# Kernel tuning notes

Measured on AMD Instinct MI355X. Metric: run time of the kernel, lower is better.

Reference implementation:

```python
import jax, jax.numpy as jnp
import numpy as np

N = 100000   # nodes
E = 3200000  # edges (avg degree 32)
G = 512      # graphs in batch
IN = 128     # in_channels
H1, C1 = 8, 8  # conv1 heads, per-head channels
OUT = 64     # out_channels (conv2, 1 head)
NEG_SLOPE = 0.2


def setup_inputs() -> dict:
    key = jax.random.key(0)
    ks = jax.random.split(key, 12)
    s = 0.1
    return dict(
        x=jax.random.normal(ks[0], (N, IN), jnp.float32),
        edge_index=jax.random.randint(ks[1], (2, E), 0, N),
        batch=jnp.sort(jax.random.randint(ks[2], (N,), 0, G)),
        W1=jax.random.normal(ks[3], (IN, H1 * C1), jnp.float32) * s,
        att_src1=jax.random.normal(ks[4], (H1, C1), jnp.float32) * s,
        att_dst1=jax.random.normal(ks[5], (H1, C1), jnp.float32) * s,
        b1=jnp.zeros((H1 * C1,), jnp.float32),
        W2=jax.random.normal(ks[6], (H1 * C1, OUT), jnp.float32) * s,
        att_src2=jax.random.normal(ks[7], (1, OUT), jnp.float32) * s,
        att_dst2=jax.random.normal(ks[8], (1, OUT), jnp.float32) * s,
        b2=jnp.zeros((OUT,), jnp.float32),
        lw1=jax.random.normal(ks[9], (OUT, 128), jnp.float32) * s,
        lb1=jnp.zeros((128,), jnp.float32),
        lw2=jax.random.normal(ks[10], (128, 1), jnp.float32) * s,
        lb2=jnp.zeros((1,), jnp.float32),
    )


def gat_layer(x, src, dst, W, a_src, a_dst, bias, heads, outc):
    # PyG GATConv (eval mode): linear -> per-edge leaky_relu attention ->
    # segment softmax over incoming edges per dst -> weighted scatter-add.
    n = x.shape[0]
    h = (x @ W).reshape(n, heads, outc)                      # [N,H,C]
    a_s = jnp.einsum('nhc,hc->nh', h, a_src)                 # [N,H]
    a_d = jnp.einsum('nhc,hc->nh', h, a_dst)
    e = jax.nn.leaky_relu(a_s[src] + a_d[dst], NEG_SLOPE)    # [E',H]
    m = jax.ops.segment_max(e, dst, num_segments=n)
    m = jax.lax.stop_gradient(jnp.where(jnp.isfinite(m), m, 0.0))
    ex = jnp.exp(e - m[dst])
    denom = jax.ops.segment_sum(ex, dst, num_segments=n)
    alpha = ex / jnp.maximum(denom[dst], 1e-16)              # [E',H]
    out = jax.ops.segment_sum(h[src] * alpha[:, :, None], dst, num_segments=n)
    return out.reshape(n, heads * outc) + bias


def reference(x, W1, att_src1, att_dst1, b1, W2, att_src2, att_dst2, b2,
              lw1, lb1, lw2, lb2, edge_index, batch):
    n = x.shape[0]
    loops = jnp.arange(n)                                    # add_self_loops=True
    src = jnp.concatenate([edge_index[0], loops])
    dst = jnp.concatenate([edge_index[1], loops])
    h = jax.nn.elu(gat_layer(x, src, dst, W1, att_src1, att_dst1, b1, H1, C1))
    h = gat_layer(h, src, dst, W2, att_src2, att_dst2, b2, 1, OUT)  # [N,OUT]
    # global_mean_pool
    s = jax.ops.segment_sum(h, batch, num_segments=G)
    cnt = jax.ops.segment_sum(jnp.ones((n, 1), h.dtype), batch, num_segments=G)
    g = s / jnp.maximum(cnt, 1.0)                            # [G,OUT]
    g = jax.nn.elu(g @ lw1 + lb1)
    return g @ lw2 + lb2                                     # [G,1]
```

## Files before the change

kernel.cpp:

```cpp
#include <hip/hip_runtime.h>
#include <hip/hip_fp16.h>
#include <math.h>

#define NN   100000
#define EE   3200000
#define GG   512
#define INC  128
#define D1   64
#define OUTC 64
#define HID  128
#define NEG  0.2f

#define BINS   782
#define BNODE  128
#define BSHIFT 7
#define BMASK  127
#define BCAP   4800
#define BKBLK 1563
#define NGB 391

typedef __attribute__((ext_vector_type(2))) float v2f;


__global__ __launch_bounds__(256, 3)
void k_fused(const int* __restrict__ srcv, const int* __restrict__ dstv,
             int* __restrict__ cursor, int* __restrict__ bucket,
             const float* __restrict__ x, const float* __restrict__ W1,
             const float* __restrict__ att_s, const float* __restrict__ att_d,
             unsigned int* __restrict__ rec, float* __restrict__ a_d) {
    __shared__ __align__(16) char smem[49152];
    int tid = threadIdx.x;
    if (blockIdx.x < NGB) {
        float4* sW4 = (float4*)smem;
        float (*sxT)[256] = (float(*)[256])(smem + 32768);
        const float4* W4 = (const float4*)W1;
        for (int i = tid; i < 128 * 16; i += 256) sW4[i] = W4[i];
        int node0 = blockIdx.x * 256;
        int rg = tid >> 3, cg = tid & 7;
        float acc[8][8];
#pragma unroll
        for (int ii = 0; ii < 8; ++ii)
#pragma unroll
            for (int jj = 0; jj < 8; ++jj) acc[ii][jj] = 0.f;
        const float4* x4 = (const float4*)x;
        for (int kt = 0; kt < 8; ++kt) {
            if (kt) __syncthreads();
#pragma unroll
            for (int q = 0; q < 4; ++q) {
                int i = q * 256 + tid;
                int r = i >> 2, kc = i & 3;
                int gn = node0 + r;
                float4 v = {0.f, 0.f, 0.f, 0.f};
                if (gn < NN) v = x4[(size_t)gn * 32 + kt * 4 + kc];
                int cs = r ^ (kc << 3);
                sxT[kc * 4 + 0][cs] = v.x;
                sxT[kc * 4 + 1][cs] = v.y;
                sxT[kc * 4 + 2][cs] = v.z;
                sxT[kc * 4 + 3][cs] = v.w;
            }
            __syncthreads();
#pragma unroll 4
            for (int kk = 0; kk < 16; ++kk) {
                int sw = (kk >> 2) << 3;
                const float* xr = &sxT[kk][(rg * 8) ^ sw];
                float4 xa = *(const float4*)xr;
                float4 xb = *(const float4*)(xr + 4);
                int kg = kt * 16 + kk;
                float4 wa = sW4[kg * 16 + cg * 2];
                float4 wb = sW4[kg * 16 + cg * 2 + 1];
                float xv[8] = {xa.x, xa.y, xa.z, xa.w, xb.x, xb.y, xb.z, xb.w};
                float wv[8] = {wa.x, wa.y, wa.z, wa.w, wb.x, wb.y, wb.z, wb.w};
#pragma unroll
                for (int ii = 0; ii < 8; ++ii)
#pragma unroll
                    for (int jj = 0; jj < 8; ++jj)
                        acc[ii][jj] = fmaf(xv[ii], wv[jj], acc[ii][jj]);
            }
        }
        float4 s0 = ((const float4*)att_s)[cg * 2];
        float4 s1 = ((const float4*)att_s)[cg * 2 + 1];
        float4 d0 = ((const float4*)att_d)[cg * 2];
        float4 d1 = ((const float4*)att_d)[cg * 2 + 1];
        uint2* hp2 = (uint2*)rec;
        __half* ash = (__half*)rec;
#pragma unroll
        for (int ii = 0; ii < 8; ++ii) {
            int n = node0 + rg * 8 + ii;
            if (n < NN) {
                float* a = acc[ii];
                int p0 = __builtin_amdgcn_cvt_pk_fp8_f32(a[0], a[1], 0, false);
                p0 = __builtin_amdgcn_cvt_pk_fp8_f32(a[2], a[3], p0, true);
                int p1 = __builtin_amdgcn_cvt_pk_fp8_f32(a[4], a[5], 0, false);
                p1 = __builtin_amdgcn_cvt_pk_fp8_f32(a[6], a[7], p1, true);
                uint2 pk; pk.x = (unsigned)p0; pk.y = (unsigned)p1;
                hp2[n * 16 + cg] = pk;
                float as = a[0] * s0.x;
                as = fmaf(a[1], s0.y, as); as = fmaf(a[2], s0.z, as);
                as = fmaf(a[3], s0.w, as); as = fmaf(a[4], s1.x, as);
                as = fmaf(a[5], s1.y, as); as = fmaf(a[6], s1.z, as);
                as = fmaf(a[7], s1.w, as);
                float ad = a[0] * d0.x;
                ad = fmaf(a[1], d0.y, ad); ad = fmaf(a[2], d0.z, ad);
                ad = fmaf(a[3], d0.w, ad); ad = fmaf(a[4], d1.x, ad);
                ad = fmaf(a[5], d1.y, ad); ad = fmaf(a[6], d1.z, ad);
                ad = fmaf(a[7], d1.w, ad);
                ash[n * 64 + 32 + cg] = __float2half(as);
                a_d[n * 8 + cg] = ad;
            }
        }
    } else {
        int* hcnt  = (int*)smem;
        int* hbase = hcnt + BINS;
        for (int i = tid; i < BINS; i += 256) hcnt[i] = 0;
        __syncthreads();
        int e0 = (blockIdx.x - NGB) * 2048;
        int bn[8], rk[8], pk[8];
#pragma unroll
        for (int q = 0; q < 8; ++q) {
            int e = e0 + q * 256 + tid;
            if (e < EE) {
                int s = srcv[e], d = dstv[e];
                bn[q] = d >> BSHIFT;
                pk[q] = (s << BSHIFT) | (d & BMASK);
                rk[q] = atomicAdd(&hcnt[bn[q]], 1);
            } else bn[q] = -1;
        }
        __syncthreads();
        for (int i = tid; i < BINS; i += 256) {
            int c = hcnt[i];
            hbase[i] = c ? atomicAdd(&cursor[i], c) : 0;
        }
        __syncthreads();
#pragma unroll
        for (int q = 0; q < 8; ++q) {
            if (bn[q] >= 0) {
                int p = hbase[bn[q]] + rk[q];
                if (p < BCAP) bucket[bn[q] * BCAP + p] = pk[q];
            }
        }
    }
}

__global__ __launch_bounds__(256)
void k_binCSR(const int* __restrict__ cursor, const int* __restrict__ bucket,
              int* __restrict__ col, int* __restrict__ rbeg, int* __restrict__ rend) {
    __shared__ int cnt_[BNODE];
    __shared__ int tmp[BNODE];
    __shared__ int cur[BNODE];
    int b = blockIdx.x, tid = threadIdx.x;
    if (tid < BNODE) cnt_[tid] = 0;
    __syncthreads();
    int m = cursor[b]; if (m > BCAP) m = BCAP;
    const int* seg = bucket + b * BCAP;
    for (int i = tid; i < m; i += 256)
        atomicAdd(&cnt_[seg[i] & BMASK], 1);
    __syncthreads();
    if (tid < BNODE) tmp[tid] = cnt_[tid];
    __syncthreads();
    for (int off = 1; off < BNODE; off <<= 1) {
        int t = (tid >= off && tid < BNODE) ? tmp[tid - off] : 0;
        __syncthreads();
        if (tid < BNODE) tmp[tid] += t;
        __syncthreads();
    }
    if (tid < BNODE) {
        int excl = tmp[tid] - cnt_[tid];
        int n = b * BNODE + tid;
        if (n < NN) {
            rbeg[n] = b * BCAP + excl;
            rend[n] = b * BCAP + excl + cnt_[tid];
        }
        cur[tid] = excl;
    }
    __syncthreads();
    for (int i = tid; i < m; i += 256) {
        int pkv = seg[i];
        int r = atomicAdd(&cur[pkv & BMASK], 1);
        col[b * BCAP + r] = pkv >> BSHIFT;
    }
}

__global__ __launch_bounds__(256, 8)
void k_gat_agg1(const int* __restrict__ rbeg, const int* __restrict__ rend,
                const int* __restrict__ col,
                const unsigned int* __restrict__ rec, const float* __restrict__ a_d,
                const float* __restrict__ b1, float* __restrict__ out) {
    int wv = threadIdx.x >> 6;
    int lane = threadIdx.x & 63;
    int half = lane >> 5;
    int d = blockIdx.x * 8 + wv * 2 + half;
    int gs = (lane >> 3) & 3;
    int l = lane & 7;
    int rb = rbeg[d], re = rend[d];
    float adh = a_d[d * 8 + l];
    const uint2* hp = (const uint2*)rec;
    const __half* asr = (const __half*)rec;
    uint2 rself = hp[d * 16 + l];
    float asself = __half2float(asr[d * 64 + 32 + l]);
    float ac[8] = {0.f,0.f,0.f,0.f,0.f,0.f,0.f,0.f};
    float denom = 0.f;
    int e = rb + gs;
    int s[4];
#pragma unroll
    for (int q = 0; q < 4; ++q) s[q] = col[e + 4 * q];
    for (; e + 12 < re; ) {
        uint2 rr[4]; float asv[4]; int sn[4];
#pragma unroll
        for (int q = 0; q < 4; ++q) rr[q] = hp[(unsigned)(s[q] * 16 + l)];
#pragma unroll
        for (int q = 0; q < 4; ++q) asv[q] = __half2float(asr[(unsigned)(s[q] * 64 + 32 + l)]);
        int en = e + 16;
#pragma unroll
        for (int q = 0; q < 4; ++q) sn[q] = col[en + 4 * q];
#pragma unroll
        for (int q = 0; q < 4; ++q) {
            float xx = asv[q] + adh;
            xx = xx >= 0.f ? xx : NEG * xx;
            float w = __expf(xx);
            denom += w;
            v2f f0 = __builtin_amdgcn_cvt_pk_f32_fp8((int)rr[q].x, false);
            v2f f1 = __builtin_amdgcn_cvt_pk_f32_fp8((int)rr[q].x, true);
            v2f f2 = __builtin_amdgcn_cvt_pk_f32_fp8((int)rr[q].y, false);
            v2f f3 = __builtin_amdgcn_cvt_pk_f32_fp8((int)rr[q].y, true);
            ac[0] = fmaf(f0.x, w, ac[0]); ac[1] = fmaf(f0.y, w, ac[1]);
            ac[2] = fmaf(f1.x, w, ac[2]); ac[3] = fmaf(f1.y, w, ac[3]);
            ac[4] = fmaf(f2.x, w, ac[4]); ac[5] = fmaf(f2.y, w, ac[5]);
            ac[6] = fmaf(f3.x, w, ac[6]); ac[7] = fmaf(f3.y, w, ac[7]);
        }
        e = en;
#pragma unroll
        for (int q = 0; q < 4; ++q) s[q] = sn[q];
    }
    for (; e < re; e += 4) {
        int s0 = col[e];
        uint2 r0 = hp[(unsigned)(s0 * 16 + l)];
        float x0 = __half2float(asr[(unsigned)(s0 * 64 + 32 + l)]) + adh;
        x0 = x0 >= 0.f ? x0 : NEG * x0;
        float w0 = __expf(x0);
        denom += w0;
        v2f f0 = __builtin_amdgcn_cvt_pk_f32_fp8((int)r0.x, false);
        v2f f1 = __builtin_amdgcn_cvt_pk_f32_fp8((int)r0.x, true);
        v2f f2 = __builtin_amdgcn_cvt_pk_f32_fp8((int)r0.y, false);
        v2f f3 = __builtin_amdgcn_cvt_pk_f32_fp8((int)r0.y, true);
        ac[0] = fmaf(f0.x, w0, ac[0]); ac[1] = fmaf(f0.y, w0, ac[1]);
        ac[2] = fmaf(f1.x, w0, ac[2]); ac[3] = fmaf(f1.y, w0, ac[3]);
        ac[4] = fmaf(f2.x, w0, ac[4]); ac[5] = fmaf(f2.y, w0, ac[5]);
        ac[6] = fmaf(f3.x, w0, ac[6]); ac[7] = fmaf(f3.y, w0, ac[7]);
    }
    if (gs == 0) {
        float es = asself + adh;
        es = es >= 0.f ? es : NEG * es;
        float w = __expf(es);
        denom += w;
        v2f f0 = __builtin_amdgcn_cvt_pk_f32_fp8((int)rself.x, false);
        v2f f1 = __builtin_amdgcn_cvt_pk_f32_fp8((int)rself.x, true);
        v2f f2 = __builtin_amdgcn_cvt_pk_f32_fp8((int)rself.y, false);
        v2f f3 = __builtin_amdgcn_cvt_pk_f32_fp8((int)rself.y, true);
        ac[0] = fmaf(f0.x, w, ac[0]); ac[1] = fmaf(f0.y, w, ac[1]);
        ac[2] = fmaf(f1.x, w, ac[2]); ac[3] = fmaf(f1.y, w, ac[3]);
        ac[4] = fmaf(f2.x, w, ac[4]); ac[5] = fmaf(f2.y, w, ac[5]);
        ac[6] = fmaf(f3.x, w, ac[6]); ac[7] = fmaf(f3.y, w, ac[7]);
    }
#pragma unroll
    for (int i = 0; i < 8; ++i) {
        ac[i] += __shfl_xor(ac[i], 8, 64);
        ac[i] += __shfl_xor(ac[i], 16, 64);
    }
    denom += __shfl_xor(denom, 8, 64);
    denom += __shfl_xor(denom, 16, 64);
    if (gs == 0) {
        float inv = 1.0f / denom;
        float4 b0 = ((const float4*)b1)[l * 2];
        float4 b4 = ((const float4*)b1)[l * 2 + 1];
        float4 r0, r1;
        r0.x = fmaf(ac[0], inv, b0.x); r0.x = r0.x > 0.f ? r0.x : expm1f(r0.x);
        r0.y = fmaf(ac[1], inv, b0.y); r0.y = r0.y > 0.f ? r0.y : expm1f(r0.y);
        r0.z = fmaf(ac[2], inv, b0.z); r0.z = r0.z > 0.f ? r0.z : expm1f(r0.z);
        r0.w = fmaf(ac[3], inv, b0.w); r0.w = r0.w > 0.f ? r0.w : expm1f(r0.w);
        r1.x = fmaf(ac[4], inv, b4.x); r1.x = r1.x > 0.f ? r1.x : expm1f(r1.x);
        r1.y = fmaf(ac[5], inv, b4.y); r1.y = r1.y > 0.f ? r1.y : expm1f(r1.y);
        r1.z = fmaf(ac[6], inv, b4.z); r1.z = r1.z > 0.f ? r1.z : expm1f(r1.z);
        r1.w = fmaf(ac[7], inv, b4.w); r1.w = r1.w > 0.f ? r1.w : expm1f(r1.w);
        ((float4*)out)[d * 16 + l * 2]     = r0;
        ((float4*)out)[d * 16 + l * 2 + 1] = r1;
    }
}

__global__ __launch_bounds__(256, 3)
void k_lin2(const float* __restrict__ hin, const float* __restrict__ W2,
            const float* __restrict__ att_s, const float* __restrict__ att_d,
            unsigned int* __restrict__ rec, float* __restrict__ a_d) {
    __shared__ float4 sW4[D1 * 16];
    __shared__ float sxT[32][256];
    int tid = threadIdx.x;
    const float4* W4 = (const float4*)W2;
    for (int i = tid; i < D1 * 16; i += 256) sW4[i] = W4[i];
    int node0 = blockIdx.x * 256;
    int rg = tid >> 3, cg = tid & 7;
    float acc[8][8];
#pragma unroll
    for (int ii = 0; ii < 8; ++ii)
#pragma unroll
        for (int jj = 0; jj < 8; ++jj) acc[ii][jj] = 0.f;
    const float4* x4 = (const float4*)hin;
    for (int kt = 0; kt < 2; ++kt) {
        if (kt) __syncthreads();
#pragma unroll
        for (int q = 0; q < 8; ++q) {
            int i = q * 256 + tid;
            int r = i >> 3, kc = i & 7;
            int gn = node0 + r;
            float4 v = {0.f, 0.f, 0.f, 0.f};
            if (gn < NN) v = x4[(size_t)gn * 16 + kt * 8 + kc];
            int cs = r ^ (kc << 3);
            sxT[kc * 4 + 0][cs] = v.x;
            sxT[kc * 4 + 1][cs] = v.y;
            sxT[kc * 4 + 2][cs] = v.z;
            sxT[kc * 4 + 3][cs] = v.w;
        }
        __syncthreads();
#pragma unroll 4
        for (int kk = 0; kk < 32; ++kk) {
            int sw = (kk >> 2) << 3;
            const float* xr = &sxT[kk][(rg * 8) ^ sw];
            float4 xa = *(const float4*)xr;
            float4 xb = *(const float4*)(xr + 4);
            int kg = kt * 32 + kk;
            float4 wa = sW4[kg * 16 + cg * 2];
            float4 wb = sW4[kg * 16 + cg * 2 + 1];
            float xv[8] = {xa.x, xa.y, xa.z, xa.w, xb.x, xb.y, xb.z, xb.w};
            float wv[8] = {wa.x, wa.y, wa.z, wa.w, wb.x, wb.y, wb.z, wb.w};
#pragma unroll
            for (int ii = 0; ii < 8; ++ii)
#pragma unroll
                for (int jj = 0; jj < 8; ++jj)
                    acc[ii][jj] = fmaf(xv[ii], wv[jj], acc[ii][jj]);
        }
    }
    float4 s0 = ((const float4*)att_s)[cg * 2];
    float4 s1 = ((const float4*)att_s)[cg * 2 + 1];
    float4 d0 = ((const float4*)att_d)[cg * 2];
    float4 d1 = ((const float4*)att_d)[cg * 2 + 1];
    uint2* hp2 = (uint2*)rec;
#pragma unroll
    for (int ii = 0; ii < 8; ++ii) {
        int n = node0 + rg * 8 + ii;
        if (n < NN) {
            float* a = acc[ii];
            int p0 = __builtin_amdgcn_cvt_pk_fp8_f32(a[0], a[1], 0, false);
            p0 = __builtin_amdgcn_cvt_pk_fp8_f32(a[2], a[3], p0, true);
            int p1 = __builtin_amdgcn_cvt_pk_fp8_f32(a[4], a[5], 0, false);
            p1 = __builtin_amdgcn_cvt_pk_fp8_f32(a[6], a[7], p1, true);
            uint2 pk; pk.x = (unsigned)p0; pk.y = (unsigned)p1;
            hp2[n * 16 + cg] = pk;
            float vs = a[0] * s0.x;
            vs = fmaf(a[1], s0.y, vs); vs = fmaf(a[2], s0.z, vs);
            vs = fmaf(a[3], s0.w, vs); vs = fmaf(a[4], s1.x, vs);
            vs = fmaf(a[5], s1.y, vs); vs = fmaf(a[6], s1.z, vs);
            vs = fmaf(a[7], s1.w, vs);
            float vd = a[0] * d0.x;
            vd = fmaf(a[1], d0.y, vd); vd = fmaf(a[2], d0.z, vd);
            vd = fmaf(a[3], d0.w, vd); vd = fmaf(a[4], d1.x, vd);
            vd = fmaf(a[5], d1.y, vd); vd = fmaf(a[6], d1.z, vd);
            vd = fmaf(a[7], d1.w, vd);
            vs += __shfl_xor(vs, 1, 64); vs += __shfl_xor(vs, 2, 64);
            vs += __shfl_xor(vs, 4, 64);
            vd += __shfl_xor(vd, 1, 64); vd += __shfl_xor(vd, 2, 64);
            vd += __shfl_xor(vd, 4, 64);
            if (cg == 0) {
                ((float*)rec)[(size_t)n * 32 + 16] = vs;
                a_d[n] = vd;
            }
        }
    }
}

__global__ __launch_bounds__(256, 8)
void k_gat_agg2(const int* __restrict__ rbeg, const int* __restrict__ rend,
                const int* __restrict__ col,
                const unsigned int* __restrict__ rec, const float* __restrict__ a_d,
                const float* __restrict__ b2, const int* __restrict__ batch,
                float* __restrict__ pool, float* __restrict__ cnt) {
    __shared__ float sv[8][64];
    __shared__ int sgi[8];
    int wv = threadIdx.x >> 6;
    int lane = threadIdx.x & 63;
    int half = lane >> 5;
    int idx = wv * 2 + half;
    int d = blockIdx.x * 8 + idx;
    int gs = (lane >> 3) & 3;
    int l = lane & 7;
    int rb = rbeg[d], re = rend[d];
    float ad = a_d[d];
    const uint2* hp = (const uint2*)rec;
    const float* recf = (const float*)rec;
    uint2 rself = hp[d * 16 + l];
    float asself = recf[d * 32 + 16];
    if (gs == 0 && l == 0) sgi[idx] = batch[d];
    float ac[8] = {0.f,0.f,0.f,0.f,0.f,0.f,0.f,0.f};
    float denom = 0.f;
    int e = rb + gs;
    int s[4];
#pragma unroll
    for (int q = 0; q < 4; ++q) s[q] = col[e + 4 * q];
    for (; e + 12 < re; ) {
        uint2 rr[4]; float asv[4]; int sn[4];
#pragma unroll
        for (int q = 0; q < 4; ++q) rr[q] = hp[(unsigned)(s[q] * 16 + l)];
#pragma unroll
        for (int q = 0; q < 4; ++q) asv[q] = recf[(unsigned)(s[q] * 32 + 16)];
        int en = e + 16;
#pragma unroll
        for (int q = 0; q < 4; ++q) sn[q] = col[en + 4 * q];
#pragma unroll
        for (int q = 0; q < 4; ++q) {
            float xx = asv[q] + ad;
            xx = xx >= 0.f ? xx : NEG * xx;
            float w = __expf(xx);
            denom += w;
            v2f f0 = __builtin_amdgcn_cvt_pk_f32_fp8((int)rr[q].x, false);
            v2f f1 = __builtin_amdgcn_cvt_pk_f32_fp8((int)rr[q].x, true);
            v2f f2 = __builtin_amdgcn_cvt_pk_f32_fp8((int)rr[q].y, false);
            v2f f3 = __builtin_amdgcn_cvt_pk_f32_fp8((int)rr[q].y, true);
            ac[0] = fmaf(f0.x, w, ac[0]); ac[1] = fmaf(f0.y, w, ac[1]);
            ac[2] = fmaf(f1.x, w, ac[2]); ac[3] = fmaf(f1.y, w, ac[3]);
            ac[4] = fmaf(f2.x, w, ac[4]); ac[5] = fmaf(f2.y, w, ac[5]);
            ac[6] = fmaf(f3.x, w, ac[6]); ac[7] = fmaf(f3.y, w, ac[7]);
        }
        e = en;
#pragma unroll
        for (int q = 0; q < 4; ++q) s[q] = sn[q];
    }
    for (; e < re; e += 4) {
        int s0 = col[e];
        uint2 r0 = hp[(unsigned)(s0 * 16 + l)];
        float x0 = recf[(unsigned)(s0 * 32 + 16)] + ad;
        x0 = x0 >= 0.f ? x0 : NEG * x0;
        float w0 = __expf(x0);
        denom += w0;
        v2f f0 = __builtin_amdgcn_cvt_pk_f32_fp8((int)r0.x, false);
        v2f f1 = __builtin_amdgcn_cvt_pk_f32_fp8((int)r0.x, true);
        v2f f2 = __builtin_amdgcn_cvt_pk_f32_fp8((int)r0.y, false);
        v2f f3 = __builtin_amdgcn_cvt_pk_f32_fp8((int)r0.y, true);
        ac[0] = fmaf(f0.x, w0, ac[0]); ac[1] = fmaf(f0.y, w0, ac[1]);
        ac[2] = fmaf(f1.x, w0, ac[2]); ac[3] = fmaf(f1.y, w0, ac[3]);
        ac[4] = fmaf(f2.x, w0, ac[4]); ac[5] = fmaf(f2.y, w0, ac[5]);
        ac[6] = fmaf(f3.x, w0, ac[6]); ac[7] = fmaf(f3.y, w0, ac[7]);
    }
    if (gs == 0) {
        float es = asself + ad;
        es = es >= 0.f ? es : NEG * es;
        float w = __expf(es);
        denom += w;
        v2f f0 = __builtin_amdgcn_cvt_pk_f32_fp8((int)rself.x, false);
        v2f f1 = __builtin_amdgcn_cvt_pk_f32_fp8((int)rself.x, true);
        v2f f2 = __builtin_amdgcn_cvt_pk_f32_fp8((int)rself.y, false);
        v2f f3 = __builtin_amdgcn_cvt_pk_f32_fp8((int)rself.y, true);
        ac[0] = fmaf(f0.x, w, ac[0]); ac[1] = fmaf(f0.y, w, ac[1]);
        ac[2] = fmaf(f1.x, w, ac[2]); ac[3] = fmaf(f1.y, w, ac[3]);
        ac[4] = fmaf(f2.x, w, ac[4]); ac[5] = fmaf(f2.y, w, ac[5]);
        ac[6] = fmaf(f3.x, w, ac[6]); ac[7] = fmaf(f3.y, w, ac[7]);
    }
#pragma unroll
    for (int i = 0; i < 8; ++i) {
        ac[i] += __shfl_xor(ac[i], 8, 64);
        ac[i] += __shfl_xor(ac[i], 16, 64);
    }
    denom += __shfl_xor(denom, 8, 64);
    denom += __shfl_xor(denom, 16, 64);
    if (gs == 0) {
        float inv = 1.0f / denom;
#pragma unroll
        for (int i = 0; i < 8; ++i)
            sv[idx][l * 8 + i] = fmaf(ac[i], inv, b2[l * 8 + i]);
    }
    __syncthreads();
    int tid = threadIdx.x;
    if (tid < 64) {
        float acc = sv[0][tid]; int curg = sgi[0];
        for (int r = 1; r < 8; ++r) {
            if (sgi[r] == curg) acc += sv[r][tid];
            else { atomicAdd(&pool[curg * 64 + tid], acc); curg = sgi[r]; acc = sv[r][tid]; }
        }
        atomicAdd(&pool[curg * 64 + tid], acc);
    } else if (tid == 64) {
        float c = 1.f; int curg = sgi[0];
        for (int r = 1; r < 8; ++r) {
            if (sgi[r] == curg) c += 1.f;
            else { atomicAdd(&cnt[curg], c); curg = sgi[r]; c = 1.f; }
        }
        atomicAdd(&cnt[curg], c);
    }
}

__global__ __launch_bounds__(128)
void k_mlp(const float* __restrict__ pool, const float* __restrict__ cnt,
           const float* __restrict__ lw1, const float* __restrict__ lb1,
           const float* __restrict__ lw2, const float* __restrict__ lb2,
           float* __restrict__ out) {
    __shared__ float sg[OUTC];
    __shared__ float sh[HID];
    int g = blockIdx.x, tid = threadIdx.x;
    float c = fmaxf(cnt[g], 1.0f);
    if (tid < OUTC) sg[tid] = pool[g * OUTC + tid] / c;
    __syncthreads();
    float acc = lb1[tid];
#pragma unroll 8
    for (int k = 0; k < OUTC; ++k)
        acc = fmaf(sg[k], lw1[k * HID + tid], acc);
    acc = acc > 0.f ? acc : expm1f(acc);
    sh[tid] = acc * lw2[tid];
    __syncthreads();
    for (int off = 64; off >= 1; off >>= 1) {
        if (tid < off) sh[tid] += sh[tid + off];
        __syncthreads();
    }
    if (tid == 0) out[g] = sh[0] + lb2[0];
}

extern "C" void kernel_launch(void* const* d_in, const int* in_sizes, int n_in,
                              void* d_out, int out_size, void* d_ws, size_t ws_size,
                              hipStream_t stream) {
    const float* x    = (const float*)d_in[0];
    const int*   ei   = (const int*)d_in[1];
    const int*   batch= (const int*)d_in[2];
    const float* W1   = (const float*)d_in[3];
    const float* as1  = (const float*)d_in[4];
    const float* ad1  = (const float*)d_in[5];
    const float* b1   = (const float*)d_in[6];
    const float* W2   = (const float*)d_in[7];
    const float* as2  = (const float*)d_in[8];
    const float* ad2  = (const float*)d_in[9];
    const float* b2   = (const float*)d_in[10];
    const float* lw1  = (const float*)d_in[11];
    const float* lb1  = (const float*)d_in[12];
    const float* lw2  = (const float*)d_in[13];
    const float* lb2  = (const float*)d_in[14];
    float* out = (float*)d_out;

    unsigned int* REC = (unsigned int*)d_ws;
    float* B    = (float*)(REC + (size_t)NN * 32);
    float* aD1  = B + (size_t)NN * 64;
    float* aD2  = aD1 + (size_t)NN * 8;
    float* pool = aD2 + NN;
    float* cnt  = pool + GG * 64;
    int* rbeg   = (int*)(cnt + GG);
    int* rend   = rbeg + NN;
    int* cursor = rend + NN;
    int* bucket = cursor + BINS;
    int* colv   = bucket + (size_t)BINS * BCAP;

    const int* srcv = ei;
    const int* dstv = ei + EE;

    hipMemsetAsync(cursor, 0, BINS * sizeof(int), stream);
    hipMemsetAsync(pool, 0, (size_t)(GG * 64 + GG) * sizeof(float), stream);

    k_fused<<<NGB + BKBLK, 256, 0, stream>>>(srcv, dstv, cursor, bucket,
                                             x, W1, as1, ad1, REC, aD1);
    k_binCSR<<<BINS, 256, 0, stream>>>(cursor, bucket, colv, rbeg, rend);

    k_gat_agg1<<<NN / 8, 256, 0, stream>>>(rbeg, rend, colv, REC, aD1, b1, B);

    k_lin2    <<<NGB, 256, 0, stream>>>(B, W2, as2, ad2, REC, aD2);
    k_gat_agg2<<<NN / 8, 256, 0, stream>>>(rbeg, rend, colv, REC, aD2, b2, batch, pool, cnt);

    k_mlp<<<GG, 128, 0, stream>>>(pool, cnt, lw1, lb1, lw2, lb2, out);
}
```

Measured before the change: 350.8 us.

## Replace bucketed CSR build with per-node count, scan, and atomic scatter

The CSR build changes from bucketing packed edges by 128-node bins with LDS histograms into three steps. Per-node in-degrees are counted with global atomics inside the fused kernel, a per-bin scan turns them into row offsets, and a separate kernel scatters source ids into col through per-node atomic cursors. This removes the intermediate bucket array and its second read/sort pass, but adds one more launch, a re-read of src/dst, and about 3.2M global atomics on scattered addresses twice. Edge order within a row now becomes nondeterministic.

```diff
diff --git a/kernel.cpp b/kernel.cpp
--- a/kernel.cpp
+++ b/kernel.cpp
@@ -23,8 +23,7 @@
 
 
 __global__ __launch_bounds__(256, 3)
-void k_fused(const int* __restrict__ srcv, const int* __restrict__ dstv,
-             int* __restrict__ cursor, int* __restrict__ bucket,
+void k_fused(const int* __restrict__ dstv, int* __restrict__ cnt_node,
              const float* __restrict__ x, const float* __restrict__ W1,
              const float* __restrict__ att_s, const float* __restrict__ att_d,
              unsigned int* __restrict__ rec, float* __restrict__ a_d) {
@@ -109,74 +108,65 @@
             }
         }
     } else {
-        int* hcnt  = (int*)smem;
-        int* hbase = hcnt + BINS;
-        for (int i = tid; i < BINS; i += 256) hcnt[i] = 0;
-        __syncthreads();
-        int e0 = (blockIdx.x - NGB) * 2048;
-        int bn[8], rk[8], pk[8];
-#pragma unroll
-        for (int q = 0; q < 8; ++q) {
-            int e = e0 + q * 256 + tid;
+        int base = (blockIdx.x - NGB) * 2048;
+#pragma unroll
+        for (int q = 0; q < 2; ++q) {
+            int e = base + (q * 256 + tid) * 4;
             if (e < EE) {
-                int s = srcv[e], d = dstv[e];
-                bn[q] = d >> BSHIFT;
-                pk[q] = (s << BSHIFT) | (d & BMASK);
-                rk[q] = atomicAdd(&hcnt[bn[q]], 1);
-            } else bn[q] = -1;
-        }
-        __syncthreads();
-        for (int i = tid; i < BINS; i += 256) {
-            int c = hcnt[i];
-            hbase[i] = c ? atomicAdd(&cursor[i], c) : 0;
-        }
-        __syncthreads();
-#pragma unroll
-        for (int q = 0; q < 8; ++q) {
-            if (bn[q] >= 0) {
-                int p = hbase[bn[q]] + rk[q];
-                if (p < BCAP) bucket[bn[q] * BCAP + p] = pk[q];
+                int4 dd = *(const int4*)(dstv + e);
+                atomicAdd(&cnt_node[dd.x], 1);
+                atomicAdd(&cnt_node[dd.y], 1);
+                atomicAdd(&cnt_node[dd.z], 1);
+                atomicAdd(&cnt_node[dd.w], 1);
             }
         }
     }
 }
 
-__global__ __launch_bounds__(256)
-void k_binCSR(const int* __restrict__ cursor, const int* __restrict__ bucket,
-              int* __restrict__ col, int* __restrict__ rbeg, int* __restrict__ rend) {
-    __shared__ int cnt_[BNODE];
+__global__ __launch_bounds__(128)
+void k_scan(const int* __restrict__ cnt_node, int* __restrict__ rbeg,
+            int* __restrict__ rend, int* __restrict__ cur) {
     __shared__ int tmp[BNODE];
-    __shared__ int cur[BNODE];
     int b = blockIdx.x, tid = threadIdx.x;
-    if (tid < BNODE) cnt_[tid] = 0;
-    __syncthreads();
-    int m = cursor[b]; if (m > BCAP) m = BCAP;
-    const int* seg = bucket + b * BCAP;
-    for (int i = tid; i < m; i += 256)
-        atomicAdd(&cnt_[seg[i] & BMASK], 1);
-    __syncthreads();
-    if (tid < BNODE) tmp[tid] = cnt_[tid];
+    int n = b * BNODE + tid;
+    int c = cnt_node[n];
+    tmp[tid] = c;
     __syncthreads();
     for (int off = 1; off < BNODE; off <<= 1) {
-        int t = (tid >= off && tid < BNODE) ? tmp[tid - off] : 0;
+        int t = (tid >= off) ? tmp[tid - off] : 0;
         __syncthreads();
-        if (tid < BNODE) tmp[tid] += t;
+        tmp[tid] += t;
         __syncthreads();
     }
-    if (tid < BNODE) {
-        int excl = tmp[tid] - cnt_[tid];
-        int n = b * BNODE + tid;
-        if (n < NN) {
-            rbeg[n] = b * BCAP + excl;
-            rend[n] = b * BCAP + excl + cnt_[tid];
-        }
-        cur[tid] = excl;
-    }
-    __syncthreads();
-    for (int i = tid; i < m; i += 256) {
-        int pkv = seg[i];
-        int r = atomicAdd(&cur[pkv & BMASK], 1);
-        col[b * BCAP + r] = pkv >> BSHIFT;
+    if (n < NN) {
+        int lim = b * BCAP + BCAP;
+        int rb = b * BCAP + (tmp[tid] - c);
+        if (rb > lim) rb = lim;
+        int re = rb + c; if (re > lim) re = lim;
+        rbeg[n] = rb; rend[n] = re; cur[n] = rb;
+    }
+}
+
+__global__ __launch_bounds__(256)
+void k_scatter(const int* __restrict__ srcv, const int* __restrict__ dstv,
+               int* __restrict__ cur, int* __restrict__ col) {
+    int tid = threadIdx.x;
+    int base = blockIdx.x * 2048;
+#pragma unroll
+    for (int q = 0; q < 2; ++q) {
+        int e = base + (q * 256 + tid) * 4;
+        if (e < EE) {
+            int4 ss = *(const int4*)(srcv + e);
+            int4 dd = *(const int4*)(dstv + e);
+            int p0 = atomicAdd(&cur[dd.x], 1);
+            if (p0 < ((dd.x >> BSHIFT) + 1) * BCAP) col[p0] = ss.x;
+            int p1 = atomicAdd(&cur[dd.y], 1);
+            if (p1 < ((dd.y >> BSHIFT) + 1) * BCAP) col[p1] = ss.y;
+            int p2 = atomicAdd(&cur[dd.z], 1);
+            if (p2 < ((dd.z >> BSHIFT) + 1) * BCAP) col[p2] = ss.z;
+            int p3 = atomicAdd(&cur[dd.w], 1);
+            if (p3 < ((dd.w >> BSHIFT) + 1) * BCAP) col[p3] = ss.w;
+        }
     }
 }
 
@@ -543,27 +533,28 @@
     float* aD1  = B + (size_t)NN * 64;
     float* aD2  = aD1 + (size_t)NN * 8;
     float* pool = aD2 + NN;
-    float* cnt  = pool + GG * 64;
-    int* rbeg   = (int*)(cnt + GG);
+    float* cntp = pool + GG * 64;
+    int* rbeg   = (int*)(cntp + GG);
     int* rend   = rbeg + NN;
-    int* cursor = rend + NN;
-    int* bucket = cursor + BINS;
-    int* colv   = bucket + (size_t)BINS * BCAP;
+    int* curv   = rend + NN;
+    int* cntn   = curv + NN;
+    int* colv   = cntn + (size_t)BINS * BNODE;
 
     const int* srcv = ei;
     const int* dstv = ei + EE;
 
-    hipMemsetAsync(cursor, 0, BINS * sizeof(int), stream);
+    hipMemsetAsync(cntn, 0, (size_t)BINS * BNODE * sizeof(int), stream);
     hipMemsetAsync(pool, 0, (size_t)(GG * 64 + GG) * sizeof(float), stream);
 
-    k_fused<<<NGB + BKBLK, 256, 0, stream>>>(srcv, dstv, cursor, bucket,
+    k_fused<<<NGB + BKBLK, 256, 0, stream>>>(dstv, cntn,
                                              x, W1, as1, ad1, REC, aD1);
-    k_binCSR<<<BINS, 256, 0, stream>>>(cursor, bucket, colv, rbeg, rend);
+    k_scan   <<<BINS, 128, 0, stream>>>(cntn, rbeg, rend, curv);
+    k_scatter<<<BKBLK, 256, 0, stream>>>(srcv, dstv, curv, colv);
 
     k_gat_agg1<<<NN / 8, 256, 0, stream>>>(rbeg, rend, colv, REC, aD1, b1, B);
 
     k_lin2    <<<NGB, 256, 0, stream>>>(B, W2, as2, ad2, REC, aD2);
-    k_gat_agg2<<<NN / 8, 256, 0, stream>>>(rbeg, rend, colv, REC, aD2, b2, batch, pool, cnt);
-
-    k_mlp<<<GG, 128, 0, stream>>>(pool, cnt, lw1, lb1, lw2, lb2, out);
-}
+    k_gat_agg2<<<NN / 8, 256, 0, stream>>>(rbeg, rend, colv, REC, aD2, b2, batch, pool, cntp);
+
+    k_mlp<<<GG, 128, 0, stream>>>(pool, cntp, lw1, lb1, lw2, lb2, out);
+}
```

New measurement: 687.5 us. 1.96x slower.
